# Optimization experiments

Hardware: AMD Instinct MI355X
Metric: run time of the kernel (lower is better)

## Reference

```python
import jax, jax.numpy as jnp
import numpy as np

B, D, C, K = 8192, 2048, 4096, 1000  # batch, input_dim, num_centers, num_classes


def setup_inputs() -> dict:
    key = jax.random.key(0)
    k0, k1, k2 = jax.random.split(key, 3)
    x = jax.random.normal(k0, (B, D), dtype=jnp.float32)
    centers = jax.random.normal(k1, (C, D), dtype=jnp.float32)
    beta = jnp.ones((C,), dtype=jnp.float32)
    W = jax.random.normal(k2, (K, C), dtype=jnp.float32) * 0.02  # fc.weight
    b = jnp.zeros((K,), dtype=jnp.float32)  # fc.bias
    return {"x": x, "centers": centers, "beta": beta, "W": W, "b": b}


def reference(x, centers, beta, W, b):
    # Pairwise Euclidean distance via the Gram trick (same math as
    # torch.norm(x[:,None,:] - centers, dim=2), without the (B,C,D) intermediate).
    x2 = jnp.sum(x * x, axis=-1, keepdims=True)          # (B, 1)
    c2 = jnp.sum(centers * centers, axis=-1)             # (C,)
    sq = x2 + c2[None, :] - 2.0 * (x @ centers.T)        # (B, C) squared distances
    dist = jnp.sqrt(jnp.maximum(sq, 0.0))
    act = jnp.exp(-beta[None, :] * dist)                 # RBF activations
    act = act / jnp.sum(act, axis=1, keepdims=True)      # normalize over centers
    return act @ W.T + b                                 # linear head (B, K)
```

## Files before the change

### kernel.cpp

```cpp
#include <hip/hip_runtime.h>


#define BB 8192
#define DD 2048
#define CC 4096
#define KK 1000
#define KP 1024

typedef unsigned short u16;
typedef __bf16 bf16x8 __attribute__((ext_vector_type(8)));
typedef float f32x4 __attribute__((ext_vector_type(4)));

typedef const void __attribute__((address_space(1)))* gvp_t;
typedef void __attribute__((address_space(3)))* lvp_t;

__device__ __forceinline__ u16 f2bf(float f) {
  union { float f; unsigned u; } v; v.f = f;
  return (u16)((v.u + 0x7fffu + ((v.u >> 16) & 1u)) >> 16);
}

__global__ void prep_all(const float* __restrict__ x, const float* __restrict__ cen,
                         const float* __restrict__ W,
                         u16* __restrict__ xb, u16* __restrict__ cb,
                         u16* __restrict__ wb,
                         float* __restrict__ x2, float* __restrict__ c2) {
  int row = blockIdx.x;
  int t = threadIdx.x;
  if (row >= BB + CC) {
    int r = row - BB - CC;
    ushort4* dst = reinterpret_cast<ushort4*>(wb + (size_t)r * CC);
    if (r < KK) {
      const float4* src = reinterpret_cast<const float4*>(W + (size_t)r * CC);
#pragma unroll
      for (int m = 0; m < 4; ++m) {
        float4 v = src[t + 256 * m];
        dst[t + 256 * m] = make_ushort4(f2bf(v.x), f2bf(v.y), f2bf(v.z), f2bf(v.w));
      }
    } else {
#pragma unroll
      for (int m = 0; m < 4; ++m) dst[t + 256 * m] = make_ushort4(0, 0, 0, 0);
    }
    return;
  }
  const float* src;
  u16* dst;
  float* nrm;
  if (row < BB) {
    src = x + (size_t)row * DD; dst = xb + (size_t)row * DD; nrm = x2 + row;
  } else {
    int r = row - BB;
    src = cen + (size_t)r * DD; dst = cb + (size_t)r * DD; nrm = c2 + r;
  }
  float s = 0.f;
#pragma unroll
  for (int m = 0; m < 2; ++m) {
    int idx = t + 256 * m;
    float4 v = reinterpret_cast<const float4*>(src)[idx];
    s += v.x * v.x + v.y * v.y + v.z * v.z + v.w * v.w;
    reinterpret_cast<ushort4*>(dst)[idx] =
        make_ushort4(f2bf(v.x), f2bf(v.y), f2bf(v.z), f2bf(v.w));
  }
#pragma unroll
  for (int off = 1; off < 64; off <<= 1) s += __shfl_xor(s, off);
  __shared__ float red[4];
  if ((t & 63) == 0) red[t >> 6] = s;
  __syncthreads();
  if (t == 0) *nrm = red[0] + red[1] + red[2] + red[3];
}

#define SB0 __builtin_amdgcn_sched_barrier(0)
#define BARR __builtin_amdgcn_s_barrier()
#define LGKM0 asm volatile("s_waitcnt lgkmcnt(0)" ::: "memory")


#define ST_A(BUF, H, TILE)                                                         \
  {                                                                                \
    const u16* _s = gA0 + (size_t)((H) * 128) * DD + (TILE) * 64;                  \
    char* _d = (char*)smem + (BUF) * 65536 + (H) * 16384 + t * 16;                 \
    __builtin_amdgcn_global_load_lds((gvp_t)_s, (lvp_t)_d, 16, 0, 0);              \
    __builtin_amdgcn_global_load_lds((gvp_t)(_s + (size_t)64 * DD),                \
                                     (lvp_t)(_d + 8192), 16, 0, 0);                \
  }

#define ST_B(BUF, H, TILE)                                                         \
  {                                                                                \
    const u16* _s = gB0 + (size_t)((H) * 128) * DD + (TILE) * 64;                  \
    char* _d = (char*)smem + (BUF) * 65536 + 32768 + (H) * 16384 + t * 16;         \
    __builtin_amdgcn_global_load_lds((gvp_t)_s, (lvp_t)_d, 16, 0, 0);              \
    __builtin_amdgcn_global_load_lds((gvp_t)(_s + (size_t)64 * DD),                \
                                     (lvp_t)(_d + 8192), 16, 0, 0);                \
  }

#define READ_B(SBP)                                                                \
  _Pragma("unroll") for (int n_ = 0; n_ < 4; ++n_) {                               \
    _Pragma("unroll") for (int ks_ = 0; ks_ < 2; ++ks_) {                          \
      bfr[n_][ks_] = *(const bf16x8*)((SBP) + bRow + n_ * 2048 + cbv[ks_]);        \
    }                                                                              \
  }

#define READ_A(SAP, MQ)                                                            \
  _Pragma("unroll") for (int m_ = 0; m_ < 2; ++m_) {                               \
    _Pragma("unroll") for (int ks_ = 0; ks_ < 2; ++ks_) {                          \
      af[m_][ks_] =                                                                \
          *(const bf16x8*)((SAP) + aRow + ((MQ)*2 + m_) * 2048 + cbv[ks_]);        \
    }                                                                              \
  }

#define MFMA_Q(MQ)                                                                 \
  __builtin_amdgcn_s_setprio(1);                                                   \
  _Pragma("unroll") for (int m_ = 0; m_ < 2; ++m_) {                               \
    _Pragma("unroll") for (int n_ = 0; n_ < 4; ++n_) {                             \
      _Pragma("unroll") for (int ks_ = 0; ks_ < 2; ++ks_) {                        \
        acc[(MQ)*2 + m_][n_] = __builtin_amdgcn_mfma_f32_16x16x32_bf16(            \
            af[m_][ks_], bfr[n_][ks_], acc[(MQ)*2 + m_][n_], 0, 0, 0);             \
      }                                                                            \
    }                                                                              \
  }                                                                                \
  __builtin_amdgcn_s_setprio(0)

#define TILE_BODY(TILE, CUR, DOA, DOB, VMN)                                        \
  {                                                                                \
    const char* sA_ = (const char*)smem + (CUR) * 65536;                           \
    const char* sB_ = sA_ + 32768;                                                 \
    READ_B(sB_);                                                                   \
    READ_A(sA_, 0);                                                                \
    SB0;                                                                           \
    if (DOA) { ST_A(1 - (CUR), 0, (TILE) + 1); ST_A(1 - (CUR), 1, (TILE) + 1); }   \
    SB0; BARR; LGKM0; SB0;                                                         \
    MFMA_Q(0); SB0; BARR;                                                          \
    READ_A(sA_, 1); SB0;                                                           \
    if (DOB) { ST_B((CUR), 0, (TILE) + 2); }                                       \
    SB0; BARR; LGKM0; SB0;                                                         \
    MFMA_Q(1); SB0; BARR;                                                          \
    READ_A(sA_, 2); SB0;                                                           \
    if (DOB) { ST_B((CUR), 1, (TILE) + 2); }                                       \
    SB0; BARR; LGKM0; SB0;                                                         \
    MFMA_Q(2); SB0; BARR;                                                          \
    READ_A(sA_, 3); SB0; BARR; LGKM0; SB0;                                         \
    MFMA_Q(3);                                                                     \
    if ((VMN) == 4) { asm volatile("s_waitcnt vmcnt(4)" ::: "memory"); }           \
    else if ((VMN) == 0) { asm volatile("s_waitcnt vmcnt(0)" ::: "memory"); }      \
    SB0; BARR;                                                                     \
  }

__global__ __launch_bounds__(512, 2)
void gemm1_rbf(const u16* __restrict__ Abf, const u16* __restrict__ Bbf,
               const float* __restrict__ x2, const float* __restrict__ c2,
               const float* __restrict__ beta, u16* __restrict__ Ebf) {
  constexpr int NT = DD / 64;
  __shared__ __align__(16) char smem[131072];

  const int t = threadIdx.x;
  const int lane = t & 63;
  const int wave = t >> 6;
  const int wr = wave >> 2;
  const int wc = wave & 3;
  const int l15 = lane & 15;

  const int rowBase = blockIdx.y * 256;
  const int colBase = blockIdx.x * 256;

  f32x4 acc[8][4];
#pragma unroll
  for (int i = 0; i < 8; ++i)
#pragma unroll
    for (int j = 0; j < 4; ++j) acc[i][j] = 0.f;

  const int srow = t >> 3;
  const u16* gA0 = Abf + (size_t)(rowBase + srow) * DD + ((t & 7) ^ (srow & 7)) * 8;
  const u16* gB0 = Bbf + (size_t)(colBase + srow) * DD + ((t & 7) ^ (srow & 7)) * 8;

  int cbv[2];
  cbv[0] = (((lane >> 4) & 3) ^ (lane & 7)) << 4;
  cbv[1] = ((4 + ((lane >> 4) & 3)) ^ (lane & 7)) << 4;
  const int aRow = (wr * 128 + l15) * 128;
  const int bRow = (wc * 64 + l15) * 128;

  bf16x8 bfr[4][2];
  bf16x8 af[2][2];

  ST_A(0, 0, 0); ST_A(0, 1, 0); ST_B(0, 0, 0); ST_B(0, 1, 0);
  ST_B(1, 0, 1); ST_B(1, 1, 1);
  asm volatile("s_waitcnt vmcnt(4)" ::: "memory");
  BARR;

#pragma unroll 2
  for (int tile = 0; tile < NT - 2; ++tile) {
    TILE_BODY(tile, tile & 1, true, true, 4);
  }
  TILE_BODY(NT - 2, (NT - 2) & 1, true, false, 0);
  TILE_BODY(NT - 1, (NT - 1) & 1, false, false, -1);

  const int khi4 = (lane >> 4) * 4;
  float c2v[4], bet[4];
  int gc[4];
#pragma unroll
  for (int n = 0; n < 4; ++n) {
    gc[n] = colBase + wc * 64 + n * 16 + l15;
    c2v[n] = c2[gc[n]];
    bet[n] = beta[gc[n]];
  }
#pragma unroll
  for (int m = 0; m < 8; ++m) {
#pragma unroll
    for (int r = 0; r < 4; ++r) {
      const int grow = rowBase + wr * 128 + m * 16 + khi4 + r;
      const float x2v = x2[grow];
      u16* orow = Ebf + (size_t)grow * CC;
#pragma unroll
      for (int n = 0; n < 4; ++n) {
        float d = acc[m][n][r];
        float sq = fmaxf(x2v + c2v[n] - 2.0f * d, 0.0f);
        float e = __expf(-bet[n] * __builtin_amdgcn_sqrtf(sq));
        orow[gc[n]] = f2bf(e);
      }
    }
  }
}


#define ST2_A(BUF, H, TILE)                                                        \
  {                                                                                \
    const u16* _s = gA0 + (size_t)((H) * 128) * CC + (TILE) * 64;                  \
    char* _d = (char*)smem + (BUF) * 49152 + (H) * 16384 + t * 16;                 \
    __builtin_amdgcn_global_load_lds((gvp_t)_s, (lvp_t)_d, 16, 0, 0);              \
    __builtin_amdgcn_global_load_lds((gvp_t)(_s + (size_t)64 * CC),                \
                                     (lvp_t)(_d + 8192), 16, 0, 0);                \
  }

#define ST2_B(BUF, TILE)                                                           \
  {                                                                                \
    const u16* _s = gB0 + (TILE) * 64;                                             \
    char* _d = (char*)smem + (BUF) * 49152 + 32768 + t * 16;                       \
    __builtin_amdgcn_global_load_lds((gvp_t)_s, (lvp_t)_d, 16, 0, 0);              \
    __builtin_amdgcn_global_load_lds((gvp_t)(_s + (size_t)64 * CC),                \
                                     (lvp_t)(_d + 8192), 16, 0, 0);                \
  }

#define READ2_B(SBP)                                                               \
  _Pragma("unroll") for (int n_ = 0; n_ < 2; ++n_) {                               \
    _Pragma("unroll") for (int ks_ = 0; ks_ < 2; ++ks_) {                          \
      bfr[n_][ks_] = *(const bf16x8*)((SBP) + bRow + n_ * 2048 + cbv[ks_]);        \
    }                                                                              \
  }

#define READ2_A(SAP, MQ)                                                           \
  _Pragma("unroll") for (int m_ = 0; m_ < 2; ++m_) {                               \
    _Pragma("unroll") for (int ks_ = 0; ks_ < 2; ++ks_) {                          \
      af[m_][ks_] =                                                                \
          *(const bf16x8*)((SAP) + aRow + ((MQ)*2 + m_) * 2048 + cbv[ks_]);        \
    }                                                                              \
  }

#define MFMA2_Q(MQ)                                                                \
  __builtin_amdgcn_s_setprio(1);                                                   \
  _Pragma("unroll") for (int m_ = 0; m_ < 2; ++m_) {                               \
    _Pragma("unroll") for (int n_ = 0; n_ < 2; ++n_) {                             \
      _Pragma("unroll") for (int ks_ = 0; ks_ < 2; ++ks_) {                        \
        acc[(MQ)*2 + m_][n_] = __builtin_amdgcn_mfma_f32_16x16x32_bf16(            \
            af[m_][ks_], bfr[n_][ks_], acc[(MQ)*2 + m_][n_], 0, 0, 0);             \
      }                                                                            \
    }                                                                              \
  }                                                                                \
  _Pragma("unroll") for (int m_ = 0; m_ < 2; ++m_) {                               \
    _Pragma("unroll") for (int ks_ = 0; ks_ < 2; ++ks_) {                          \
      rsacc[(MQ)*2 + m_] = __builtin_amdgcn_mfma_f32_16x16x32_bf16(                \
          af[m_][ks_], onesf, rsacc[(MQ)*2 + m_], 0, 0, 0);                        \
    }                                                                              \
  }                                                                                \
  __builtin_amdgcn_s_setprio(0)

#define TILE2_BODY(TILE, CUR, DOA, DOB, VMN)                                       \
  {                                                                                \
    const char* sA_ = (const char*)smem + (CUR) * 49152;                           \
    const char* sB_ = sA_ + 32768;                                                 \
    READ2_B(sB_);                                                                  \
    READ2_A(sA_, 0);                                                               \
    SB0;                                                                           \
    if (DOA) { ST2_A(1 - (CUR), 0, (TILE) + 1); }                                  \
    SB0; BARR; LGKM0; SB0;                                                         \
    MFMA2_Q(0); SB0; BARR;                                                         \
    READ2_A(sA_, 1); SB0;                                                          \
    if (DOA) { ST2_A(1 - (CUR), 1, (TILE) + 1); }                                  \
    SB0; BARR; LGKM0; SB0;                                                         \
    MFMA2_Q(1); SB0; BARR;                                                         \
    READ2_A(sA_, 2); SB0;                                                          \
    if (DOB) { ST2_B((CUR), (TILE) + 2); }                                         \
    SB0; BARR; LGKM0; SB0;                                                         \
    MFMA2_Q(2); SB0; BARR;                                                         \
    READ2_A(sA_, 3); SB0; BARR; LGKM0; SB0;                                        \
    MFMA2_Q(3);                                                                    \
    if ((VMN) == 2) { asm volatile("s_waitcnt vmcnt(2)" ::: "memory"); }           \
    else if ((VMN) == 0) { asm volatile("s_waitcnt vmcnt(0)" ::: "memory"); }      \
    SB0; BARR;                                                                     \
  }

__global__ __launch_bounds__(512, 2)
void gemm2_out(const u16* __restrict__ Ebf, const u16* __restrict__ Wbf,
               const float* __restrict__ bias, float* __restrict__ out) {
  constexpr int NT = CC / 64;
  __shared__ __align__(16) char smem[98304];

  const int t = threadIdx.x;
  const int lane = t & 63;
  const int wave = t >> 6;
  const int wr = wave >> 2;
  const int wc = wave & 3;
  const int l15 = lane & 15;

  const int rowBase = blockIdx.y * 256;
  const int colBase = blockIdx.x * 128;

  f32x4 acc[8][2];
#pragma unroll
  for (int i = 0; i < 8; ++i)
#pragma unroll
    for (int j = 0; j < 2; ++j) acc[i][j] = 0.f;

  f32x4 rsacc[8];
#pragma unroll
  for (int i = 0; i < 8; ++i) rsacc[i] = 0.f;
  bf16x8 onesf;
#pragma unroll
  for (int e = 0; e < 8; ++e) onesf[e] = (__bf16)1.0f;

  const int srow = t >> 3;
  const u16* gA0 = Ebf + (size_t)(rowBase + srow) * CC + ((t & 7) ^ (srow & 7)) * 8;
  const u16* gB0 = Wbf + (size_t)(colBase + srow) * CC + ((t & 7) ^ (srow & 7)) * 8;

  int cbv[2];
  cbv[0] = (((lane >> 4) & 3) ^ (lane & 7)) << 4;
  cbv[1] = ((4 + ((lane >> 4) & 3)) ^ (lane & 7)) << 4;
  const int aRow = (wr * 128 + l15) * 128;
  const int bRow = (wc * 32 + l15) * 128;

  bf16x8 bfr[2][2];
  bf16x8 af[2][2];

  ST2_A(0, 0, 0); ST2_A(0, 1, 0); ST2_B(0, 0);
  ST2_B(1, 1);
  asm volatile("s_waitcnt vmcnt(2)" ::: "memory");
  BARR;

#pragma unroll 2
  for (int tile = 0; tile < NT - 2; ++tile) {
    TILE2_BODY(tile, tile & 1, true, true, 2);
  }
  TILE2_BODY(NT - 2, (NT - 2) & 1, true, false, 0);
  TILE2_BODY(NT - 1, (NT - 1) & 1, false, false, -1);

  const int khi4 = (lane >> 4) * 4;
  int gc[2];
  float bv[2];
#pragma unroll
  for (int n = 0; n < 2; ++n) {
    gc[n] = colBase + wc * 32 + n * 16 + l15;
    bv[n] = (gc[n] < KK) ? bias[gc[n]] : 0.f;
  }
#pragma unroll
  for (int m = 0; m < 8; ++m) {
#pragma unroll
    for (int r = 0; r < 4; ++r) {
      const int grow = rowBase + wr * 128 + m * 16 + khi4 + r;
      const float inv = 1.0f / rsacc[m][r];
#pragma unroll
      for (int n = 0; n < 2; ++n) {
        if (gc[n] < KK)
          out[(size_t)grow * KK + gc[n]] = acc[m][n][r] * inv + bv[n];
      }
    }
  }
}

#define OFF_XB 0u
#define OFF_CB 33554432u
#define OFF_WB 50331648u
#define OFF_EB 58720256u
#define OFF_X2 125829120u
#define OFF_C2 125861888u

extern "C" void kernel_launch(void* const* d_in, const int* in_sizes, int n_in,
                              void* d_out, int out_size, void* d_ws, size_t ws_size,
                              hipStream_t stream) {
  const float* x = (const float*)d_in[0];
  const float* cen = (const float*)d_in[1];
  const float* beta = (const float*)d_in[2];
  const float* W = (const float*)d_in[3];
  const float* bias = (const float*)d_in[4];
  float* out = (float*)d_out;
  char* ws = (char*)d_ws;

  u16* xb = (u16*)(ws + OFF_XB);
  u16* cb = (u16*)(ws + OFF_CB);
  u16* wb = (u16*)(ws + OFF_WB);
  u16* eb = (u16*)(ws + OFF_EB);
  float* x2 = (float*)(ws + OFF_X2);
  float* c2 = (float*)(ws + OFF_C2);

  prep_all<<<BB + CC + KP, 256, 0, stream>>>(x, cen, W, xb, cb, wb, x2, c2);
  gemm1_rbf<<<dim3(CC / 256, BB / 256), 512, 0, stream>>>(xb, cb, x2, c2, beta, eb);
  gemm2_out<<<dim3(KP / 128, BB / 256), 512, 0, stream>>>(eb, wb, bias, out);
}
```

Baseline: 354.5 us.

## Compute RBF row sums in gemm1 epilogue and remodel gemm2 block order

The row normalization sum moves out of gemm2's extra ones-vector MFMAs and into gemm1's epilogue. There each wave reduces its partial sums with shuffles and writes them to a scratch buffer that aliases the output. A small reduce kernel then produces per-row sums, which gemm2 reads in its epilogue, cutting MFMA work in gemm2's inner loop. gemm2 also remaps block indices so blocks sharing W columns and E rows run close together for better L2 reuse. The cost is an extra launch, the partial-sum writes, and summing fp32 values before the bf16 rounding, which differs slightly from summing the rounded values.

```diff
diff --git a/kernel.cpp b/kernel.cpp
--- a/kernel.cpp
+++ b/kernel.cpp
@@ -123,7 +123,7 @@
     const char* sA_ = (const char*)smem + (CUR) * 65536;                           \
     const char* sB_ = sA_ + 32768;                                                 \
     READ_B(sB_);                                                                   \
-    READ_A(sA_, 0);                                                                \
+    READ_A(sA_, 0);                                                               \
     SB0;                                                                           \
     if (DOA) { ST_A(1 - (CUR), 0, (TILE) + 1); ST_A(1 - (CUR), 1, (TILE) + 1); }   \
     SB0; BARR; LGKM0; SB0;                                                         \
@@ -146,7 +146,8 @@
 __global__ __launch_bounds__(512, 2)
 void gemm1_rbf(const u16* __restrict__ Abf, const u16* __restrict__ Bbf,
                const float* __restrict__ x2, const float* __restrict__ c2,
-               const float* __restrict__ beta, u16* __restrict__ Ebf) {
+               const float* __restrict__ beta, u16* __restrict__ Ebf,
+               float* __restrict__ psum) {
   constexpr int NT = DD / 64;
   __shared__ __align__(16) char smem[131072];
 
@@ -192,6 +193,7 @@
   TILE_BODY(NT - 1, (NT - 1) & 1, false, false, -1);
 
   const int khi4 = (lane >> 4) * 4;
+  const int pslot = (blockIdx.x << 2) + wc;
   float c2v[4], bet[4];
   int gc[4];
 #pragma unroll
@@ -207,15 +209,32 @@
       const int grow = rowBase + wr * 128 + m * 16 + khi4 + r;
       const float x2v = x2[grow];
       u16* orow = Ebf + (size_t)grow * CC;
+      float rs = 0.f;
 #pragma unroll
       for (int n = 0; n < 4; ++n) {
         float d = acc[m][n][r];
         float sq = fmaxf(x2v + c2v[n] - 2.0f * d, 0.0f);
         float e = __expf(-bet[n] * __builtin_amdgcn_sqrtf(sq));
+        rs += e;
         orow[gc[n]] = f2bf(e);
       }
+#pragma unroll
+      for (int off = 1; off < 16; off <<= 1) rs += __shfl_xor(rs, off);
+      if (l15 == 0) psum[(size_t)grow * 64 + pslot] = rs;
     }
   }
+}
+
+__global__ void rowsum_reduce(const float* __restrict__ psum, float* __restrict__ rowsum) {
+  const int row = blockIdx.x * 256 + threadIdx.x;
+  const float4* p = reinterpret_cast<const float4*>(psum + (size_t)row * 64);
+  float s = 0.f;
+#pragma unroll
+  for (int i = 0; i < 16; ++i) {
+    float4 v = p[i];
+    s += v.x + v.y + v.z + v.w;
+  }
+  rowsum[row] = s;
 }
 
 
@@ -262,12 +281,6 @@
       }                                                                            \
     }                                                                              \
   }                                                                                \
-  _Pragma("unroll") for (int m_ = 0; m_ < 2; ++m_) {                               \
-    _Pragma("unroll") for (int ks_ = 0; ks_ < 2; ++ks_) {                          \
-      rsacc[(MQ)*2 + m_] = __builtin_amdgcn_mfma_f32_16x16x32_bf16(                \
-          af[m_][ks_], onesf, rsacc[(MQ)*2 + m_], 0, 0, 0);                        \
-    }                                                                              \
-  }                                                                                \
   __builtin_amdgcn_s_setprio(0)
 
 #define TILE2_BODY(TILE, CUR, DOA, DOB, VMN)                                       \
@@ -297,7 +310,8 @@
 
 __global__ __launch_bounds__(512, 2)
 void gemm2_out(const u16* __restrict__ Ebf, const u16* __restrict__ Wbf,
-               const float* __restrict__ bias, float* __restrict__ out) {
+               const float* __restrict__ rowsum, const float* __restrict__ bias,
+               float* __restrict__ out) {
   constexpr int NT = CC / 64;
   __shared__ __align__(16) char smem[98304];
 
@@ -308,21 +322,19 @@
   const int wc = wave & 3;
   const int l15 = lane & 15;
 
-  const int rowBase = blockIdx.y * 256;
-  const int colBase = blockIdx.x * 128;
+  const int d = blockIdx.x + (blockIdx.y << 3);
+  const int s_ = d >> 3;
+  const int by = (d & 7) + ((s_ >> 3) << 3);
+  const int bx = s_ & 7;
+
+  const int rowBase = by * 256;
+  const int colBase = bx * 128;
 
   f32x4 acc[8][2];
 #pragma unroll
   for (int i = 0; i < 8; ++i)
 #pragma unroll
     for (int j = 0; j < 2; ++j) acc[i][j] = 0.f;
-
-  f32x4 rsacc[8];
-#pragma unroll
-  for (int i = 0; i < 8; ++i) rsacc[i] = 0.f;
-  bf16x8 onesf;
-#pragma unroll
-  for (int e = 0; e < 8; ++e) onesf[e] = (__bf16)1.0f;
 
   const int srow = t >> 3;
   const u16* gA0 = Ebf + (size_t)(rowBase + srow) * CC + ((t & 7) ^ (srow & 7)) * 8;
@@ -362,7 +374,7 @@
 #pragma unroll
     for (int r = 0; r < 4; ++r) {
       const int grow = rowBase + wr * 128 + m * 16 + khi4 + r;
-      const float inv = 1.0f / rsacc[m][r];
+      const float inv = 1.0f / rowsum[grow];
 #pragma unroll
       for (int n = 0; n < 2; ++n) {
         if (gc[n] < KK)
@@ -378,6 +390,7 @@
 #define OFF_EB 58720256u
 #define OFF_X2 125829120u
 #define OFF_C2 125861888u
+#define OFF_RS 125878272u
 
 extern "C" void kernel_launch(void* const* d_in, const int* in_sizes, int n_in,
                               void* d_out, int out_size, void* d_ws, size_t ws_size,
@@ -396,8 +409,11 @@
   u16* eb = (u16*)(ws + OFF_EB);
   float* x2 = (float*)(ws + OFF_X2);
   float* c2 = (float*)(ws + OFF_C2);
+  float* rowsum = (float*)(ws + OFF_RS);
+  float* psum = out;
 
   prep_all<<<BB + CC + KP, 256, 0, stream>>>(x, cen, W, xb, cb, wb, x2, c2);
-  gemm1_rbf<<<dim3(CC / 256, BB / 256), 512, 0, stream>>>(xb, cb, x2, c2, beta, eb);
-  gemm2_out<<<dim3(KP / 128, BB / 256), 512, 0, stream>>>(eb, wb, bias, out);
-}
+  gemm1_rbf<<<dim3(CC / 256, BB / 256), 512, 0, stream>>>(xb, cb, x2, c2, beta, eb, psum);
+  rowsum_reduce<<<BB / 256, 256, 0, stream>>>(psum, rowsum);
+  gemm2_out<<<dim3(KP / 128, BB / 256), 512, 0, stream>>>(eb, wb, rowsum, bias, out);
+}
```

Result: faster. 345.7 us (-2.5%).
